# Kernel optimization log

Measured on AMD Instinct MI355X. Metric: run time of the kernel, lower is better.

## Reference

```python
import jax, jax.numpy as jnp
import numpy as np

C = 1.0          # Poincare ball curvature
NORM_FACTOR = 1.0
EPS = 1e-7
MAX_NORM = (1.0 - 1e-5) / np.sqrt(C)


def _artanh(x):
    x = jnp.clip(x, -1.0 + EPS, 1.0 - EPS)
    return jnp.arctanh(x)


def logmap0(x):
    # tangent vector at origin of Poincare ball (c=C)
    n = jnp.clip(jnp.linalg.norm(x, axis=-1, keepdims=True), EPS, None)
    sc = np.sqrt(C)
    return _artanh(sc * n) * x / (sc * n)


def expmap0(u):
    n = jnp.clip(jnp.linalg.norm(u, axis=-1, keepdims=True), EPS, None)
    sc = np.sqrt(C)
    return jnp.tanh(sc * n) * u / (sc * n)


def proj(x):
    # clip points to stay strictly inside the ball
    n = jnp.clip(jnp.linalg.norm(x, axis=-1, keepdims=True), EPS, None)
    return jnp.where(n > MAX_NORM, x / n * MAX_NORM, x)


def setup_inputs() -> dict:
    key = jax.random.key(0)
    ks = jax.random.split(key, 10)
    B, N, D_IN, D_H, D_LAT, L = 32, 1024, 128, 128, 64, 2
    s_in = 1.0 / np.sqrt(D_IN)
    s_h = 1.0 / np.sqrt(D_H)
    return {
        "node_features": jax.random.normal(ks[0], (B, N, D_IN), jnp.float32),
        "adjacency_matrix": jax.random.uniform(ks[1], (B, N, N), jnp.float32),
        "node_mask": jnp.ones((B, N, 1), jnp.float32),
        "W_embed": jax.random.normal(ks[2], (D_H, D_IN), jnp.float32) * s_in,
        "W_msg": jax.random.normal(ks[3], (L, D_H, D_H), jnp.float32) * s_h,
        "b_msg": jnp.zeros((L, D_H), jnp.float32),
        "W_agg": jax.random.normal(ks[4], (L, D_H, D_H), jnp.float32) * s_h,
        "b_agg": jnp.zeros((L, D_H), jnp.float32),
        "W_proj": jax.random.normal(ks[5], (2 * D_LAT, D_H), jnp.float32) * s_h,
        "b_proj": jnp.zeros((2 * D_LAT,), jnp.float32),
    }


def reference(node_features, adjacency_matrix, node_mask,
              W_embed, W_msg, b_msg, W_agg, b_agg, W_proj, b_proj):
    # feature embedding (bias-free linear, weights live on the manifold);
    # map to the Poincare ball
    h = jnp.einsum('bnd,hd->bnh', node_features, W_embed)
    x = proj(expmap0(h))

    num_layers = W_msg.shape[0]
    for l in range(num_layers):  # small fixed layer count
        t = logmap0(x)                                   # [B,N,D]
        m = t @ W_msg[l] + b_msg[l]                      # message transform
        agg = jnp.einsum('bij,bjd->bid', adjacency_matrix, m) / NORM_FACTOR
        agg = agg @ W_agg[l] + b_agg[l]                  # aggregation transform
        t = jax.nn.relu(m + agg)                         # tangent-space activation
        x = proj(expmap0(t))

    tangent = logmap0(x)                                 # final logmap0 in encode()
    mean_logvar = tangent @ W_proj.T + b_proj            # [B,N,2*latent]
    return mean_logvar * node_mask
```

## Files before the change

### kernel.cpp

```cpp
#include <hip/hip_runtime.h>
#include <hip/hip_bf16.h>

typedef __bf16 bf16;
typedef __bf16 bf16x8 __attribute__((ext_vector_type(8)));
typedef float  floatx4 __attribute__((ext_vector_type(4)));

#define EPSF    1e-7f
#define MAXNORM 0.99999f
#define TS_LD   136

__device__ __forceinline__ float hyp_scale(float ss) {
    float n  = sqrtf(ss);
    float nh = fmaxf(n, EPSF);
    float s1 = tanhf(nh) / nh;
    float nx = s1 * n;
    if (nx > MAXNORM) { s1 *= MAXNORM / nx; nx = MAXNORM; }
    float nx2 = fmaxf(nx, EPSF);
    return (atanhf(nx2) / nx2) * s1;
}

__device__ __forceinline__ bf16x8 cvt8(float4 a, float4 b) {
    bf16x8 r;
    r[0] = (bf16)a.x; r[1] = (bf16)a.y; r[2] = (bf16)a.z; r[3] = (bf16)a.w;
    r[4] = (bf16)b.x; r[5] = (bf16)b.y; r[6] = (bf16)b.z; r[7] = (bf16)b.w;
    return r;
}

__device__ __forceinline__ int sw128(int row, int k) {
    return row * 128 + (((k >> 3) ^ (row & 15)) << 3) + (k & 7);
}
__device__ __forceinline__ int sw64(int row, int k) {
    return row * 64 + (((k >> 3) ^ (row & 7)) << 3) + (k & 7);
}

__global__ __launch_bounds__(256) void embed_msg(
    const float* __restrict__ X, const float* __restrict__ Wemb,
    const float* __restrict__ Wmsg, const float* __restrict__ bmsg,
    bf16* __restrict__ M, bf16* __restrict__ MT)
{
    __shared__ __align__(16) bf16 Xs[128 * 128];
    __shared__ __align__(16) bf16 Ws[128 * 128];
    __shared__ __align__(16) bf16 W2[128 * 128];
    __shared__ __align__(16) bf16 Ts[128 * TS_LD];
    const int tid = threadIdx.x, bx = blockIdx.x;

    {
        const float4* Xg = reinterpret_cast<const float4*>(X + (size_t)bx * 16384);
        #pragma unroll
        for (int i = 0; i < 8; ++i) {
            int g = tid + i * 256, row = g >> 4, gc = g & 15;
            float4 v0 = Xg[2 * g], v1 = Xg[2 * g + 1];
            *reinterpret_cast<bf16x8*>(&Xs[row * 128 + ((gc ^ (row & 15)) << 3)]) = cvt8(v0, v1);
        }
    }
    {
        const float4* Wg = reinterpret_cast<const float4*>(Wemb);
        #pragma unroll
        for (int i = 0; i < 8; ++i) {
            int g = tid + i * 256, row = g >> 4, gc = g & 15;
            float4 v0 = Wg[2 * g], v1 = Wg[2 * g + 1];
            *reinterpret_cast<bf16x8*>(&Ws[row * 128 + ((gc ^ (row & 15)) << 3)]) = cvt8(v0, v1);
        }
    }
    {
        const int c0 = (tid & 15) * 8;
        #pragma unroll
        for (int rr = 0; rr < 8; ++rr) {
            int r = (tid >> 4) * 8 + rr;
            const float4* p = reinterpret_cast<const float4*>(Wmsg + r * 128 + c0);
            float4 v0 = p[0], v1 = p[1];
            float vv[8] = {v0.x, v0.y, v0.z, v0.w, v1.x, v1.y, v1.z, v1.w};
            #pragma unroll
            for (int j = 0; j < 8; ++j) {
                int n = c0 + j;
                W2[n * 128 + (((r >> 3) ^ (n & 15)) << 3) + (r & 7)] = (bf16)vv[j];
            }
        }
    }
    __syncthreads();

    const int lane = tid & 63, wv = tid >> 6, n16 = lane & 15, quad = lane >> 4;
    const int rbase = wv * 32;

    floatx4 acc[2][8];
    #pragma unroll
    for (int a = 0; a < 2; ++a)
        #pragma unroll
        for (int c = 0; c < 8; ++c) acc[a][c] = (floatx4){0.f, 0.f, 0.f, 0.f};
    #pragma unroll
    for (int kc = 0; kc < 4; ++kc) {
        int k0 = kc * 32 + quad * 8;
        bf16x8 a0 = *reinterpret_cast<const bf16x8*>(&Xs[sw128(rbase + n16, k0)]);
        bf16x8 a1 = *reinterpret_cast<const bf16x8*>(&Xs[sw128(rbase + 16 + n16, k0)]);
        #pragma unroll
        for (int ct = 0; ct < 8; ++ct) {
            bf16x8 b = *reinterpret_cast<const bf16x8*>(&Ws[sw128(ct * 16 + n16, k0)]);
            acc[0][ct] = __builtin_amdgcn_mfma_f32_16x16x32_bf16(a0, b, acc[0][ct], 0, 0, 0);
            acc[1][ct] = __builtin_amdgcn_mfma_f32_16x16x32_bf16(a1, b, acc[1][ct], 0, 0, 0);
        }
    }
    #pragma unroll
    for (int rt = 0; rt < 2; ++rt) {
        #pragma unroll
        for (int r = 0; r < 4; ++r) {
            int row = rbase + rt * 16 + quad * 4 + r;
            float u[8], ss = 0.f;
            #pragma unroll
            for (int ct = 0; ct < 8; ++ct) { u[ct] = acc[rt][ct][r]; ss += u[ct] * u[ct]; }
            #pragma unroll
            for (int off = 1; off < 16; off <<= 1) ss += __shfl_xor(ss, off);
            float sc = hyp_scale(ss);
            #pragma unroll
            for (int ct = 0; ct < 8; ++ct)
                Ts[row * TS_LD + ct * 16 + n16] = (bf16)(u[ct] * sc);
        }
    }
    __syncthreads();

    floatx4 acc2[2][8];
    #pragma unroll
    for (int a = 0; a < 2; ++a)
        #pragma unroll
        for (int c = 0; c < 8; ++c) acc2[a][c] = (floatx4){0.f, 0.f, 0.f, 0.f};
    #pragma unroll
    for (int kc = 0; kc < 4; ++kc) {
        int k0 = kc * 32 + quad * 8;
        bf16x8 a0 = *reinterpret_cast<const bf16x8*>(&Ts[(rbase + n16) * TS_LD + k0]);
        bf16x8 a1 = *reinterpret_cast<const bf16x8*>(&Ts[(rbase + 16 + n16) * TS_LD + k0]);
        #pragma unroll
        for (int ct = 0; ct < 8; ++ct) {
            bf16x8 b = *reinterpret_cast<const bf16x8*>(&W2[sw128(ct * 16 + n16, k0)]);
            acc2[0][ct] = __builtin_amdgcn_mfma_f32_16x16x32_bf16(a0, b, acc2[0][ct], 0, 0, 0);
            acc2[1][ct] = __builtin_amdgcn_mfma_f32_16x16x32_bf16(a1, b, acc2[1][ct], 0, 0, 0);
        }
    }
    float bv[8];
    #pragma unroll
    for (int ct = 0; ct < 8; ++ct) bv[ct] = bmsg[ct * 16 + n16];
    #pragma unroll
    for (int rt = 0; rt < 2; ++rt) {
        #pragma unroll
        for (int r = 0; r < 4; ++r) {
            int lrow = rbase + rt * 16 + quad * 4 + r;
            size_t grow = (size_t)bx * 128 + lrow;
            #pragma unroll
            for (int ct = 0; ct < 8; ++ct) {
                bf16 o = (bf16)(acc2[rt][ct][r] + bv[ct]);
                M[grow * 128 + ct * 16 + n16] = o;
                MT[((grow >> 10) * 128 + ct * 16 + n16) * 1024 + (grow & 1023)] = o;
            }
        }
    }
}

template <int LAST>
__global__ __launch_bounds__(512) void adj_fused(
    const float* __restrict__ Adj, const bf16* __restrict__ MT,
    const bf16* __restrict__ Mprev,
    const float* __restrict__ Wagg, const float* __restrict__ bagg,
    const float* __restrict__ W2f,  const float* __restrict__ b2,
    const float* __restrict__ Mask,
    bf16* __restrict__ Mout, bf16* __restrict__ MTout, float* __restrict__ Out)
{
    __shared__ __align__(16) bf16 smem[4 * 128 * 64];
    __shared__ __align__(16) bf16 Ts[128 * TS_LD];
    bf16* As0 = smem;
    bf16* As1 = smem + 128 * 64;
    bf16* Bs0 = smem + 2 * 128 * 64;
    bf16* Bs1 = smem + 3 * 128 * 64;

    const int tid = threadIdx.x, bid = blockIdx.x;
    const int mt = bid >> 5, b = bid & 31;
    const float* Ag = Adj + ((size_t)b << 20) + ((size_t)mt << 17);
    const bf16*  Bg = MT  + ((size_t)b << 17);

    const int lane = tid & 63, wv = tid >> 6, n16 = lane & 15, quad = lane >> 4;
    const int wr = (wv >> 2) * 64, wc = (wv & 3) * 32;

    const int kk0 = (bid * 5 + (bid >> 5)) & 15;

    floatx4 acc[4][2];
    #pragma unroll
    for (int a = 0; a < 4; ++a)
        #pragma unroll
        for (int c = 0; c < 2; ++c) acc[a][c] = (floatx4){0.f, 0.f, 0.f, 0.f};

    float4 pa[2][2]; bf16x8 pb[2];
    auto load_regs = [&](int kk) {
        #pragma unroll
        for (int i = 0; i < 2; ++i) {
            int g = tid + i * 512, row = g >> 3, gc = g & 7;
            const float4* pA = reinterpret_cast<const float4*>(
                Ag + (size_t)row * 1024 + kk * 64 + gc * 8);
            pa[i][0] = pA[0]; pa[i][1] = pA[1];
            pb[i] = *reinterpret_cast<const bf16x8*>(Bg + (size_t)row * 1024 + kk * 64 + gc * 8);
        }
    };
    auto store_lds = [&](bf16* A, bf16* B) {
        #pragma unroll
        for (int i = 0; i < 2; ++i) {
            int g = tid + i * 512, row = g >> 3, gc = g & 7;
            *reinterpret_cast<bf16x8*>(&A[row * 64 + ((gc ^ (row & 7)) << 3)]) = cvt8(pa[i][0], pa[i][1]);
            *reinterpret_cast<bf16x8*>(&B[row * 64 + ((gc ^ (row & 7)) << 3)]) = pb[i];
        }
    };

    load_regs(kk0);
    store_lds(As0, Bs0);
    for (int p = 0; p < 16; ++p) {
        bf16* Acur = (p & 1) ? As1 : As0;
        bf16* Bcur = (p & 1) ? Bs1 : Bs0;
        bf16* Anxt = (p & 1) ? As0 : As1;
        bf16* Bnxt = (p & 1) ? Bs0 : Bs1;
        __syncthreads();
        if (p < 15) load_regs((p + 1 + kk0) & 15);
        #pragma unroll
        for (int kc = 0; kc < 2; ++kc) {
            int ko = kc * 32 + quad * 8;
            bf16x8 a[4], bb[2];
            #pragma unroll
            for (int rt = 0; rt < 4; ++rt)
                a[rt] = *reinterpret_cast<const bf16x8*>(&Acur[sw64(wr + rt * 16 + n16, ko)]);
            #pragma unroll
            for (int ct = 0; ct < 2; ++ct)
                bb[ct] = *reinterpret_cast<const bf16x8*>(&Bcur[sw64(wc + ct * 16 + n16, ko)]);
            #pragma unroll
            for (int rt = 0; rt < 4; ++rt)
                #pragma unroll
                for (int ct = 0; ct < 2; ++ct)
                    acc[rt][ct] = __builtin_amdgcn_mfma_f32_16x16x32_bf16(a[rt], bb[ct], acc[rt][ct], 0, 0, 0);
        }
        if (p < 15) store_lds(Anxt, Bnxt);
    }
    __syncthreads();

    #pragma unroll
    for (int rt = 0; rt < 4; ++rt)
        #pragma unroll
        for (int ct = 0; ct < 2; ++ct)
            #pragma unroll
            for (int r = 0; r < 4; ++r) {
                int row = wr + rt * 16 + quad * 4 + r, col = wc + ct * 16 + n16;
                Ts[row * TS_LD + col] = (bf16)acc[rt][ct][r];
            }

    bf16* Wa = smem;
    bf16* W2 = smem + 128 * 128;
    {
        const int c0 = (tid & 15) * 8;
        #pragma unroll
        for (int rr = 0; rr < 4; ++rr) {
            int r = (tid >> 4) * 4 + rr;
            const float4* p = reinterpret_cast<const float4*>(Wagg + r * 128 + c0);
            float4 v0 = p[0], v1 = p[1];
            float vv[8] = {v0.x, v0.y, v0.z, v0.w, v1.x, v1.y, v1.z, v1.w};
            #pragma unroll
            for (int j = 0; j < 8; ++j) {
                int n = c0 + j;
                Wa[n * 128 + (((r >> 3) ^ (n & 15)) << 3) + (r & 7)] = (bf16)vv[j];
            }
        }
    }
    if (LAST) {
        const float4* Wg = reinterpret_cast<const float4*>(W2f);
        #pragma unroll
        for (int i = 0; i < 4; ++i) {
            int g = tid + i * 512, row = g >> 4, gc = g & 15;
            float4 v0 = Wg[2 * g], v1 = Wg[2 * g + 1];
            *reinterpret_cast<bf16x8*>(&W2[row * 128 + ((gc ^ (row & 15)) << 3)]) = cvt8(v0, v1);
        }
    } else {
        const int c0 = (tid & 15) * 8;
        #pragma unroll
        for (int rr = 0; rr < 4; ++rr) {
            int r = (tid >> 4) * 4 + rr;
            const float4* p = reinterpret_cast<const float4*>(W2f + r * 128 + c0);
            float4 v0 = p[0], v1 = p[1];
            float vv[8] = {v0.x, v0.y, v0.z, v0.w, v1.x, v1.y, v1.z, v1.w};
            #pragma unroll
            for (int j = 0; j < 8; ++j) {
                int n = c0 + j;
                W2[n * 128 + (((r >> 3) ^ (n & 15)) << 3) + (r & 7)] = (bf16)vv[j];
            }
        }
    }
    __syncthreads();

    const int rbase = wv * 16;
    const size_t growbase = (size_t)b * 1024 + (size_t)mt * 128;
    floatx4 acc2[8];
    #pragma unroll
    for (int c = 0; c < 8; ++c) acc2[c] = (floatx4){0.f, 0.f, 0.f, 0.f};
    #pragma unroll
    for (int kc = 0; kc < 4; ++kc) {
        int k0 = kc * 32 + quad * 8;
        bf16x8 a = *reinterpret_cast<const bf16x8*>(&Ts[(rbase + n16) * TS_LD + k0]);
        #pragma unroll
        for (int ct = 0; ct < 8; ++ct) {
            bf16x8 bb = *reinterpret_cast<const bf16x8*>(&Wa[sw128(ct * 16 + n16, k0)]);
            acc2[ct] = __builtin_amdgcn_mfma_f32_16x16x32_bf16(a, bb, acc2[ct], 0, 0, 0);
        }
    }
    {
        float bva[8];
        #pragma unroll
        for (int ct = 0; ct < 8; ++ct) bva[ct] = bagg[ct * 16 + n16];
        #pragma unroll
        for (int r = 0; r < 4; ++r) {
            int row = rbase + quad * 4 + r;
            size_t grow = growbase + row;
            float u[8], ss = 0.f;
            #pragma unroll
            for (int ct = 0; ct < 8; ++ct) {
                u[ct] = fmaxf(acc2[ct][r] + bva[ct] + (float)Mprev[grow * 128 + ct * 16 + n16], 0.f);
                ss += u[ct] * u[ct];
            }
            #pragma unroll
            for (int off = 1; off < 16; off <<= 1) ss += __shfl_xor(ss, off);
            float sc = hyp_scale(ss);
            #pragma unroll
            for (int ct = 0; ct < 8; ++ct)
                Ts[row * TS_LD + ct * 16 + n16] = (bf16)(u[ct] * sc);
        }
    }

    floatx4 acc3[8];
    #pragma unroll
    for (int c = 0; c < 8; ++c) acc3[c] = (floatx4){0.f, 0.f, 0.f, 0.f};
    #pragma unroll
    for (int kc = 0; kc < 4; ++kc) {
        int k0 = kc * 32 + quad * 8;
        bf16x8 a = *reinterpret_cast<const bf16x8*>(&Ts[(rbase + n16) * TS_LD + k0]);
        #pragma unroll
        for (int ct = 0; ct < 8; ++ct) {
            bf16x8 bb = *reinterpret_cast<const bf16x8*>(&W2[sw128(ct * 16 + n16, k0)]);
            acc3[ct] = __builtin_amdgcn_mfma_f32_16x16x32_bf16(a, bb, acc3[ct], 0, 0, 0);
        }
    }
    float bv2[8];
    #pragma unroll
    for (int ct = 0; ct < 8; ++ct) bv2[ct] = b2[ct * 16 + n16];
    #pragma unroll
    for (int r = 0; r < 4; ++r) {
        int row = rbase + quad * 4 + r;
        size_t grow = growbase + row;
        if (LAST) {
            float mk = Mask[grow];
            #pragma unroll
            for (int ct = 0; ct < 8; ++ct)
                Out[grow * 128 + ct * 16 + n16] = (acc3[ct][r] + bv2[ct]) * mk;
        } else {
            #pragma unroll
            for (int ct = 0; ct < 8; ++ct) {
                bf16 o = (bf16)(acc3[ct][r] + bv2[ct]);
                Mout[grow * 128 + ct * 16 + n16] = o;
                MTout[((grow >> 10) * 128 + ct * 16 + n16) * 1024 + (grow & 1023)] = o;
            }
        }
    }
}

extern "C" void kernel_launch(void* const* d_in, const int* in_sizes, int n_in,
                              void* d_out, int out_size, void* d_ws, size_t ws_size,
                              hipStream_t stream)
{
    const float* X    = (const float*)d_in[0];
    const float* Adj  = (const float*)d_in[1];
    const float* Mask = (const float*)d_in[2];
    const float* Wemb = (const float*)d_in[3];
    const float* Wmsg = (const float*)d_in[4];
    const float* bmsg = (const float*)d_in[5];
    const float* Wagg = (const float*)d_in[6];
    const float* bagg = (const float*)d_in[7];
    const float* Wprj = (const float*)d_in[8];
    const float* bprj = (const float*)d_in[9];
    float* out = (float*)d_out;

    const size_t BN = 32768;
    bf16* m0  = (bf16*)d_ws;
    bf16* m0T = m0  + BN * 128;
    bf16* m1  = m0T + BN * 128;
    bf16* m1T = m1  + BN * 128;

    embed_msg<<<256, 256, 0, stream>>>(X, Wemb, Wmsg, bmsg, m0, m0T);
    adj_fused<0><<<256, 512, 0, stream>>>(Adj, m0T, m0, Wagg, bagg,
                                          Wmsg + 16384, bmsg + 128, nullptr,
                                          m1, m1T, nullptr);
    adj_fused<1><<<256, 512, 0, stream>>>(Adj, m1T, m1, Wagg + 16384, bagg + 128,
                                          Wprj, bprj, Mask,
                                          nullptr, nullptr, out);
}
```

Baseline: 302.6 us.

## Pre-pack adjacency to swizzled bf16 and stream it via direct global-to-LDS loads

Adds a pack_adj kernel that converts the fp32 adjacency once into a tiled, pre-swizzled bf16 buffer in workspace. Both layer kernels then read it with global_load_lds in a three-stage pipeline, which avoids reading the fp32 adjacency twice and removes register-based conversion. The trade is an extra full fp32 read plus a bf16 write of the adjacency in the pack pass, and this path is taken only when the workspace is large enough; otherwise the old kernels run.

```diff
diff --git a/kernel.cpp b/kernel.cpp
--- a/kernel.cpp
+++ b/kernel.cpp
@@ -31,6 +31,27 @@
 }
 __device__ __forceinline__ int sw64(int row, int k) {
     return row * 64 + (((k >> 3) ^ (row & 7)) << 3) + (k & 7);
+}
+
+__device__ __forceinline__ void gl_lds16(const void* g, void* l) {
+    __builtin_amdgcn_global_load_lds(
+        (__attribute__((address_space(1))) unsigned int*)(g),
+        (__attribute__((address_space(3))) unsigned int*)(l), 16, 0, 0);
+}
+
+__global__ __launch_bounds__(256) void pack_adj(
+    const float* __restrict__ Adj, bf16* __restrict__ AdjB)
+{
+    const int t = threadIdx.x, bp = blockIdx.x;
+    #pragma unroll
+    for (int k = 0; k < 8; ++k) {
+        int G = bp * 2048 + k * 256 + t;
+        int gp = G & 7, row = (G >> 3) & 127, kk = (G >> 10) & 15, mtb = G >> 14;
+        const float4* s4 = reinterpret_cast<const float4*>(
+            Adj + ((size_t)mtb << 17) + (row << 10) + kk * 64 + ((gp ^ (row & 7)) << 3));
+        float4 v0 = s4[0], v1 = s4[1];
+        *reinterpret_cast<bf16x8*>(AdjB + (size_t)G * 8) = cvt8(v0, v1);
+    }
 }
 
 __global__ __launch_bounds__(256) void embed_msg(
@@ -148,6 +169,206 @@
                 bf16 o = (bf16)(acc2[rt][ct][r] + bv[ct]);
                 M[grow * 128 + ct * 16 + n16] = o;
                 MT[((grow >> 10) * 128 + ct * 16 + n16) * 1024 + (grow & 1023)] = o;
+            }
+        }
+    }
+}
+
+template <int LAST>
+__global__ __launch_bounds__(512) void adj_fast(
+    const bf16* __restrict__ AdjB, const bf16* __restrict__ MT,
+    const bf16* __restrict__ Mprev,
+    const float* __restrict__ Wagg, const float* __restrict__ bagg,
+    const float* __restrict__ W2f,  const float* __restrict__ b2,
+    const float* __restrict__ Mask,
+    bf16* __restrict__ Mout, bf16* __restrict__ MTout, float* __restrict__ Out)
+{
+    __shared__ __align__(16) bf16 smem[6 * 128 * 64];
+    __shared__ __align__(16) bf16 Ts[128 * TS_LD];
+
+    const int tid = threadIdx.x, bid = blockIdx.x;
+    const int mt = bid >> 5, b = bid & 31;
+    const bf16* Ab = AdjB + ((size_t)(b * 8 + mt) << 17);
+    const bf16* Bg = MT + ((size_t)b << 17);
+
+    const int lane = tid & 63, wv = tid >> 6, n16 = lane & 15, quad = lane >> 4;
+    const int wr = (wv >> 2) * 64, wc = (wv & 3) * 32;
+
+    bf16* As[3] = { smem,         smem + 8192,  smem + 16384 };
+    bf16* Bs[3] = { smem + 24576, smem + 32768, smem + 40960 };
+
+    floatx4 acc[4][2];
+    #pragma unroll
+    for (int a = 0; a < 4; ++a)
+        #pragma unroll
+        for (int c = 0; c < 2; ++c) acc[a][c] = (floatx4){0.f, 0.f, 0.f, 0.f};
+
+    auto stage = [&](int kk, bf16* Adst, bf16* Bdst) {
+        const bf16* at = Ab + (size_t)kk * 8192;
+        #pragma unroll
+        for (int j = 0; j < 2; ++j) {
+            int base = wv * 128 + j * 64;
+            gl_lds16(at + (size_t)(base + lane) * 8, Adst + base * 8);
+            int gi = base + lane;
+            int n = gi >> 3, gp = gi & 7;
+            gl_lds16(Bg + (size_t)n * 1024 + kk * 64 + ((gp ^ (n & 7)) << 3),
+                     Bdst + base * 8);
+        }
+    };
+
+    stage(0, As[0], Bs[0]);
+    stage(1, As[1], Bs[1]);
+    #pragma unroll
+    for (int p = 0; p < 16; ++p) {
+        if (p < 15) asm volatile("s_waitcnt vmcnt(4)" ::: "memory");
+        else        asm volatile("s_waitcnt vmcnt(0)" ::: "memory");
+        __builtin_amdgcn_s_barrier();
+        __builtin_amdgcn_sched_barrier(0);
+        if (p + 2 < 16) stage(p + 2, As[(p + 2) % 3], Bs[(p + 2) % 3]);
+        const bf16* Acur = As[p % 3];
+        const bf16* Bcur = Bs[p % 3];
+        #pragma unroll
+        for (int kc = 0; kc < 2; ++kc) {
+            int ko = kc * 32 + quad * 8;
+            bf16x8 a[4], bb[2];
+            #pragma unroll
+            for (int rt = 0; rt < 4; ++rt)
+                a[rt] = *reinterpret_cast<const bf16x8*>(&Acur[sw64(wr + rt * 16 + n16, ko)]);
+            #pragma unroll
+            for (int ct = 0; ct < 2; ++ct)
+                bb[ct] = *reinterpret_cast<const bf16x8*>(&Bcur[sw64(wc + ct * 16 + n16, ko)]);
+            __builtin_amdgcn_s_setprio(1);
+            #pragma unroll
+            for (int rt = 0; rt < 4; ++rt)
+                #pragma unroll
+                for (int ct = 0; ct < 2; ++ct)
+                    acc[rt][ct] = __builtin_amdgcn_mfma_f32_16x16x32_bf16(a[rt], bb[ct], acc[rt][ct], 0, 0, 0);
+            __builtin_amdgcn_s_setprio(0);
+        }
+    }
+    __syncthreads();
+
+    #pragma unroll
+    for (int rt = 0; rt < 4; ++rt)
+        #pragma unroll
+        for (int ct = 0; ct < 2; ++ct)
+            #pragma unroll
+            for (int r = 0; r < 4; ++r) {
+                int row = wr + rt * 16 + quad * 4 + r, col = wc + ct * 16 + n16;
+                Ts[row * TS_LD + col] = (bf16)acc[rt][ct][r];
+            }
+
+    bf16* Wa = smem;
+    bf16* W2 = smem + 128 * 128;
+    {
+        const int c0 = (tid & 15) * 8;
+        #pragma unroll
+        for (int rr = 0; rr < 4; ++rr) {
+            int r = (tid >> 4) * 4 + rr;
+            const float4* p = reinterpret_cast<const float4*>(Wagg + r * 128 + c0);
+            float4 v0 = p[0], v1 = p[1];
+            float vv[8] = {v0.x, v0.y, v0.z, v0.w, v1.x, v1.y, v1.z, v1.w};
+            #pragma unroll
+            for (int j = 0; j < 8; ++j) {
+                int n = c0 + j;
+                Wa[n * 128 + (((r >> 3) ^ (n & 15)) << 3) + (r & 7)] = (bf16)vv[j];
+            }
+        }
+    }
+    if (LAST) {
+        const float4* Wg = reinterpret_cast<const float4*>(W2f);
+        #pragma unroll
+        for (int i = 0; i < 4; ++i) {
+            int g = tid + i * 512, row = g >> 4, gc = g & 15;
+            float4 v0 = Wg[2 * g], v1 = Wg[2 * g + 1];
+            *reinterpret_cast<bf16x8*>(&W2[row * 128 + ((gc ^ (row & 15)) << 3)]) = cvt8(v0, v1);
+        }
+    } else {
+        const int c0 = (tid & 15) * 8;
+        #pragma unroll
+        for (int rr = 0; rr < 4; ++rr) {
+            int r = (tid >> 4) * 4 + rr;
+            const float4* p = reinterpret_cast<const float4*>(W2f + r * 128 + c0);
+            float4 v0 = p[0], v1 = p[1];
+            float vv[8] = {v0.x, v0.y, v0.z, v0.w, v1.x, v1.y, v1.z, v1.w};
+            #pragma unroll
+            for (int j = 0; j < 8; ++j) {
+                int n = c0 + j;
+                W2[n * 128 + (((r >> 3) ^ (n & 15)) << 3) + (r & 7)] = (bf16)vv[j];
+            }
+        }
+    }
+    __syncthreads();
+
+    const int rbase = wv * 16;
+    const size_t growbase = (size_t)b * 1024 + (size_t)mt * 128;
+    floatx4 acc2[8];
+    #pragma unroll
+    for (int c = 0; c < 8; ++c) acc2[c] = (floatx4){0.f, 0.f, 0.f, 0.f};
+    #pragma unroll
+    for (int kc = 0; kc < 4; ++kc) {
+        int k0 = kc * 32 + quad * 8;
+        bf16x8 a = *reinterpret_cast<const bf16x8*>(&Ts[(rbase + n16) * TS_LD + k0]);
+        #pragma unroll
+        for (int ct = 0; ct < 8; ++ct) {
+            bf16x8 bb = *reinterpret_cast<const bf16x8*>(&Wa[sw128(ct * 16 + n16, k0)]);
+            acc2[ct] = __builtin_amdgcn_mfma_f32_16x16x32_bf16(a, bb, acc2[ct], 0, 0, 0);
+        }
+    }
+    {
+        float bva[8];
+        #pragma unroll
+        for (int ct = 0; ct < 8; ++ct) bva[ct] = bagg[ct * 16 + n16];
+        #pragma unroll
+        for (int r = 0; r < 4; ++r) {
+            int row = rbase + quad * 4 + r;
+            size_t grow = growbase + row;
+            float u[8], ss = 0.f;
+            #pragma unroll
+            for (int ct = 0; ct < 8; ++ct) {
+                u[ct] = fmaxf(acc2[ct][r] + bva[ct] + (float)Mprev[grow * 128 + ct * 16 + n16], 0.f);
+                ss += u[ct] * u[ct];
+            }
+            #pragma unroll
+            for (int off = 1; off < 16; off <<= 1) ss += __shfl_xor(ss, off);
+            float sc = hyp_scale(ss);
+            #pragma unroll
+            for (int ct = 0; ct < 8; ++ct)
+                Ts[row * TS_LD + ct * 16 + n16] = (bf16)(u[ct] * sc);
+        }
+    }
+
+    floatx4 acc3[8];
+    #pragma unroll
+    for (int c = 0; c < 8; ++c) acc3[c] = (floatx4){0.f, 0.f, 0.f, 0.f};
+    #pragma unroll
+    for (int kc = 0; kc < 4; ++kc) {
+        int k0 = kc * 32 + quad * 8;
+        bf16x8 a = *reinterpret_cast<const bf16x8*>(&Ts[(rbase + n16) * TS_LD + k0]);
+        #pragma unroll
+        for (int ct = 0; ct < 8; ++ct) {
+            bf16x8 bb = *reinterpret_cast<const bf16x8*>(&W2[sw128(ct * 16 + n16, k0)]);
+            acc3[ct] = __builtin_amdgcn_mfma_f32_16x16x32_bf16(a, bb, acc3[ct], 0, 0, 0);
+        }
+    }
+    float bv2[8];
+    #pragma unroll
+    for (int ct = 0; ct < 8; ++ct) bv2[ct] = b2[ct * 16 + n16];
+    #pragma unroll
+    for (int r = 0; r < 4; ++r) {
+        int row = rbase + quad * 4 + r;
+        size_t grow = growbase + row;
+        if (LAST) {
+            float mk = Mask[grow];
+            #pragma unroll
+            for (int ct = 0; ct < 8; ++ct)
+                Out[grow * 128 + ct * 16 + n16] = (acc3[ct][r] + bv2[ct]) * mk;
+        } else {
+            #pragma unroll
+            for (int ct = 0; ct < 8; ++ct) {
+                bf16 o = (bf16)(acc3[ct][r] + bv2[ct]);
+                Mout[grow * 128 + ct * 16 + n16] = o;
+                MTout[((grow >> 10) * 128 + ct * 16 + n16) * 1024 + (grow & 1023)] = o;
             }
         }
     }
@@ -377,16 +598,30 @@
     float* out = (float*)d_out;
 
     const size_t BN = 32768;
-    bf16* m0  = (bf16*)d_ws;
-    bf16* m0T = m0  + BN * 128;
-    bf16* m1  = m0T + BN * 128;
-    bf16* m1T = m1  + BN * 128;
-
-    embed_msg<<<256, 256, 0, stream>>>(X, Wemb, Wmsg, bmsg, m0, m0T);
-    adj_fused<0><<<256, 512, 0, stream>>>(Adj, m0T, m0, Wagg, bagg,
-                                          Wmsg + 16384, bmsg + 128, nullptr,
-                                          m1, m1T, nullptr);
-    adj_fused<1><<<256, 512, 0, stream>>>(Adj, m1T, m1, Wagg + 16384, bagg + 128,
-                                          Wprj, bprj, Mask,
-                                          nullptr, nullptr, out);
-}
+    bf16* m0   = (bf16*)d_ws;
+    bf16* m0T  = m0  + BN * 128;
+    bf16* m1   = m0T + BN * 128;
+    bf16* m1T  = m1  + BN * 128;
+    bf16* AdjB = m1T + BN * 128;
+
+    const size_t need = (4 * BN * 128 + (size_t)33554432) * sizeof(bf16);
+
+    if (ws_size >= need) {
+        pack_adj<<<2048, 256, 0, stream>>>(Adj, AdjB);
+        embed_msg<<<256, 256, 0, stream>>>(X, Wemb, Wmsg, bmsg, m0, m0T);
+        adj_fast<0><<<256, 512, 0, stream>>>(AdjB, m0T, m0, Wagg, bagg,
+                                             Wmsg + 16384, bmsg + 128, nullptr,
+                                             m1, m1T, nullptr);
+        adj_fast<1><<<256, 512, 0, stream>>>(AdjB, m1T, m1, Wagg + 16384, bagg + 128,
+                                             Wprj, bprj, Mask,
+                                             nullptr, nullptr, out);
+    } else {
+        embed_msg<<<256, 256, 0, stream>>>(X, Wemb, Wmsg, bmsg, m0, m0T);
+        adj_fused<0><<<256, 512, 0, stream>>>(Adj, m0T, m0, Wagg, bagg,
+                                              Wmsg + 16384, bmsg + 128, nullptr,
+                                              m1, m1T, nullptr);
+        adj_fused<1><<<256, 512, 0, stream>>>(Adj, m1T, m1, Wagg + 16384, bagg + 128,
+                                              Wprj, bprj, Mask,
+                                              nullptr, nullptr, out);
+    }
+}
```

Measured after the change: 317.2 us. 4.8% more time.

## Pre-tile transposed messages, stage B via direct global-to-LDS loads, double grid

Applied to the files above, without the earlier changes.

Messages are now written to MT in a pre-tiled, pre-swizzled 64-column block layout, staged through LDS so the global stores are coalesced 16-byte vectors instead of scattered 2-byte transposed writes. The adjacency kernel then copies B tiles straight into LDS with global_load_lds, skipping the register round trip. Each block now covers 64 rows instead of 128, so the grid doubles to 512 blocks for better CU occupancy on a memory-bound adjacency stream. In exchange, the B tiles are loaded twice as often across blocks, and half the waves sit idle during the small dense epilogue GEMMs.

```diff
diff --git a/kernel.cpp b/kernel.cpp
--- a/kernel.cpp
+++ b/kernel.cpp
@@ -32,6 +32,13 @@
 __device__ __forceinline__ int sw64(int row, int k) {
     return row * 64 + (((k >> 3) ^ (row & 7)) << 3) + (k & 7);
 }
+
+__device__ __forceinline__ void gl_lds16(const void* g, void* l) {
+    __builtin_amdgcn_global_load_lds(
+        (__attribute__((address_space(1))) unsigned int*)(g),
+        (__attribute__((address_space(3))) unsigned int*)(l), 16, 0, 0);
+}
+
 
 __global__ __launch_bounds__(256) void embed_msg(
     const float* __restrict__ X, const float* __restrict__ Wemb,
@@ -144,17 +151,39 @@
             int lrow = rbase + rt * 16 + quad * 4 + r;
             size_t grow = (size_t)bx * 128 + lrow;
             #pragma unroll
+            for (int ct = 0; ct < 8; ++ct)
+                M[grow * 128 + ct * 16 + n16] = (bf16)(acc2[rt][ct][r] + bv[ct]);
+        }
+    }
+    __syncthreads();
+    bf16* Ts2 = W2;
+    #pragma unroll
+    for (int rt = 0; rt < 2; ++rt) {
+        #pragma unroll
+        for (int r = 0; r < 4; ++r) {
+            int lrow = rbase + rt * 16 + quad * 4 + r;
+            #pragma unroll
             for (int ct = 0; ct < 8; ++ct) {
-                bf16 o = (bf16)(acc2[rt][ct][r] + bv[ct]);
-                M[grow * 128 + ct * 16 + n16] = o;
-                MT[((grow >> 10) * 128 + ct * 16 + n16) * 1024 + (grow & 1023)] = o;
-            }
+                int dim = ct * 16 + n16;
+                Ts2[dim * 128 + (lrow ^ ((dim & 7) << 3))] = (bf16)(acc2[rt][ct][r] + bv[ct]);
+            }
+        }
+    }
+    __syncthreads();
+    {
+        const size_t tb = (((size_t)(bx >> 3) * 16 + (size_t)(bx & 7) * 2) << 10);
+        #pragma unroll
+        for (int i = 0; i < 8; ++i) {
+            int g = i * 256 + tid;
+            int gp = g & 7, n = (g >> 3) & 127, kkl = g >> 10;
+            bf16x8 v = *reinterpret_cast<const bf16x8*>(&Ts2[n * 128 + kkl * 64 + gp * 8]);
+            *reinterpret_cast<bf16x8*>(MT + ((tb + (size_t)g) << 3)) = v;
         }
     }
 }
 
 template <int LAST>
-__global__ __launch_bounds__(512) void adj_fused(
+__global__ __launch_bounds__(512) void adj_fast(
     const float* __restrict__ Adj, const bf16* __restrict__ MT,
     const bf16* __restrict__ Mprev,
     const float* __restrict__ Wagg, const float* __restrict__ bagg,
@@ -162,80 +191,84 @@
     const float* __restrict__ Mask,
     bf16* __restrict__ Mout, bf16* __restrict__ MTout, float* __restrict__ Out)
 {
-    __shared__ __align__(16) bf16 smem[4 * 128 * 64];
-    __shared__ __align__(16) bf16 Ts[128 * TS_LD];
-    bf16* As0 = smem;
-    bf16* As1 = smem + 128 * 64;
-    bf16* Bs0 = smem + 2 * 128 * 64;
-    bf16* Bs1 = smem + 3 * 128 * 64;
+    __shared__ __align__(16) bf16 smem[33280];
 
     const int tid = threadIdx.x, bid = blockIdx.x;
-    const int mt = bid >> 5, b = bid & 31;
-    const float* Ag = Adj + ((size_t)b << 20) + ((size_t)mt << 17);
-    const bf16*  Bg = MT  + ((size_t)b << 17);
+    const int h = bid >> 8, inner = bid & 255;
+    const int mt = inner >> 5, b = inner & 31;
+    const float* Ag = Adj + ((size_t)b << 20) + ((size_t)mt << 17) + ((size_t)h << 16);
+    const bf16*  Bg = MT + ((size_t)b << 17);
 
     const int lane = tid & 63, wv = tid >> 6, n16 = lane & 15, quad = lane >> 4;
-    const int wr = (wv >> 2) * 64, wc = (wv & 3) * 32;
+    const int wr = (wv >> 2) * 32, wc = (wv & 3) * 32;
 
     const int kk0 = (bid * 5 + (bid >> 5)) & 15;
 
-    floatx4 acc[4][2];
-    #pragma unroll
-    for (int a = 0; a < 4; ++a)
+    floatx4 acc[2][2];
+    #pragma unroll
+    for (int a = 0; a < 2; ++a)
         #pragma unroll
         for (int c = 0; c < 2; ++c) acc[a][c] = (floatx4){0.f, 0.f, 0.f, 0.f};
 
-    float4 pa[2][2]; bf16x8 pb[2];
+    const int arow = tid >> 3, agc = tid & 7;
+    float4 pa0, pa1;
     auto load_regs = [&](int kk) {
-        #pragma unroll
-        for (int i = 0; i < 2; ++i) {
-            int g = tid + i * 512, row = g >> 3, gc = g & 7;
-            const float4* pA = reinterpret_cast<const float4*>(
-                Ag + (size_t)row * 1024 + kk * 64 + gc * 8);
-            pa[i][0] = pA[0]; pa[i][1] = pA[1];
-            pb[i] = *reinterpret_cast<const bf16x8*>(Bg + (size_t)row * 1024 + kk * 64 + gc * 8);
-        }
+        const float4* pA = reinterpret_cast<const float4*>(
+            Ag + (size_t)arow * 1024 + kk * 64 + agc * 8);
+        pa0 = pA[0]; pa1 = pA[1];
     };
-    auto store_lds = [&](bf16* A, bf16* B) {
-        #pragma unroll
-        for (int i = 0; i < 2; ++i) {
-            int g = tid + i * 512, row = g >> 3, gc = g & 7;
-            *reinterpret_cast<bf16x8*>(&A[row * 64 + ((gc ^ (row & 7)) << 3)]) = cvt8(pa[i][0], pa[i][1]);
-            *reinterpret_cast<bf16x8*>(&B[row * 64 + ((gc ^ (row & 7)) << 3)]) = pb[i];
-        }
+    auto store_lds = [&](int slot) {
+        bf16* A = smem + slot * 4096;
+        *reinterpret_cast<bf16x8*>(&A[arow * 64 + ((agc ^ (arow & 7)) << 3)]) = cvt8(pa0, pa1);
     };
+    auto stage_b = [&](int kk, int slot) {
+        const bf16* bt = Bg + ((size_t)kk << 13);
+        bf16* Bdst = smem + 8192 + slot * 8192;
+        #pragma unroll
+        for (int j = 0; j < 2; ++j) {
+            int base = wv * 128 + j * 64;
+            gl_lds16(bt + (size_t)(base + lane) * 8, Bdst + base * 8);
+        }
+    };
 
     load_regs(kk0);
-    store_lds(As0, Bs0);
+    stage_b(kk0, 0);
+    store_lds(0);
     for (int p = 0; p < 16; ++p) {
-        bf16* Acur = (p & 1) ? As1 : As0;
-        bf16* Bcur = (p & 1) ? Bs1 : Bs0;
-        bf16* Anxt = (p & 1) ? As0 : As1;
-        bf16* Bnxt = (p & 1) ? Bs0 : Bs1;
+        const bf16* Acur = smem + (p & 1) * 4096;
+        const bf16* Bcur = smem + 8192 + (p & 1) * 8192;
         __syncthreads();
-        if (p < 15) load_regs((p + 1 + kk0) & 15);
+        if (p < 15) {
+            int nk = (p + 1 + kk0) & 15;
+            load_regs(nk);
+            stage_b(nk, (p + 1) & 1);
+        }
         #pragma unroll
         for (int kc = 0; kc < 2; ++kc) {
             int ko = kc * 32 + quad * 8;
-            bf16x8 a[4], bb[2];
-            #pragma unroll
-            for (int rt = 0; rt < 4; ++rt)
+            bf16x8 a[2], bb[2];
+            #pragma unroll
+            for (int rt = 0; rt < 2; ++rt)
                 a[rt] = *reinterpret_cast<const bf16x8*>(&Acur[sw64(wr + rt * 16 + n16, ko)]);
             #pragma unroll
             for (int ct = 0; ct < 2; ++ct)
                 bb[ct] = *reinterpret_cast<const bf16x8*>(&Bcur[sw64(wc + ct * 16 + n16, ko)]);
             #pragma unroll
-            for (int rt = 0; rt < 4; ++rt)
+            for (int rt = 0; rt < 2; ++rt)
                 #pragma unroll
                 for (int ct = 0; ct < 2; ++ct)
                     acc[rt][ct] = __builtin_amdgcn_mfma_f32_16x16x32_bf16(a[rt], bb[ct], acc[rt][ct], 0, 0, 0);
         }
-        if (p < 15) store_lds(Anxt, Bnxt);
-    }
-    __syncthreads();
-
-    #pragma unroll
-    for (int rt = 0; rt < 4; ++rt)
+        if (p < 15) store_lds((p + 1) & 1);
+    }
+    __syncthreads();
+
+    bf16* Ts  = smem;
+    bf16* Wa  = smem + 8704;
+    bf16* Ts2 = smem + 25088;
+
+    #pragma unroll
+    for (int rt = 0; rt < 2; ++rt)
         #pragma unroll
         for (int ct = 0; ct < 2; ++ct)
             #pragma unroll
@@ -243,9 +276,6 @@
                 int row = wr + rt * 16 + quad * 4 + r, col = wc + ct * 16 + n16;
                 Ts[row * TS_LD + col] = (bf16)acc[rt][ct][r];
             }
-
-    bf16* Wa = smem;
-    bf16* W2 = smem + 128 * 128;
     {
         const int c0 = (tid & 15) * 8;
         #pragma unroll
@@ -261,13 +291,54 @@
             }
         }
     }
+    __syncthreads();
+
+    const int rbase = (wv & 3) * 16;
+    const size_t growbase = (size_t)b * 1024 + (size_t)mt * 128 + (size_t)h * 64;
+    floatx4 acc2[8];
+    #pragma unroll
+    for (int c = 0; c < 8; ++c) acc2[c] = (floatx4){0.f, 0.f, 0.f, 0.f};
+    if (wv < 4) {
+        #pragma unroll
+        for (int kc = 0; kc < 4; ++kc) {
+            int k0 = kc * 32 + quad * 8;
+            bf16x8 a = *reinterpret_cast<const bf16x8*>(&Ts[(rbase + n16) * TS_LD + k0]);
+            #pragma unroll
+            for (int ct = 0; ct < 8; ++ct) {
+                bf16x8 bb = *reinterpret_cast<const bf16x8*>(&Wa[sw128(ct * 16 + n16, k0)]);
+                acc2[ct] = __builtin_amdgcn_mfma_f32_16x16x32_bf16(a, bb, acc2[ct], 0, 0, 0);
+            }
+        }
+        float bva[8];
+        #pragma unroll
+        for (int ct = 0; ct < 8; ++ct) bva[ct] = bagg[ct * 16 + n16];
+        #pragma unroll
+        for (int r = 0; r < 4; ++r) {
+            int row = rbase + quad * 4 + r;
+            size_t grow = growbase + row;
+            float u[8], ss = 0.f;
+            #pragma unroll
+            for (int ct = 0; ct < 8; ++ct) {
+                u[ct] = fmaxf(acc2[ct][r] + bva[ct] + (float)Mprev[grow * 128 + ct * 16 + n16], 0.f);
+                ss += u[ct] * u[ct];
+            }
+            #pragma unroll
+            for (int off = 1; off < 16; off <<= 1) ss += __shfl_xor(ss, off);
+            float sc = hyp_scale(ss);
+            #pragma unroll
+            for (int ct = 0; ct < 8; ++ct)
+                Ts[row * TS_LD + ct * 16 + n16] = (bf16)(u[ct] * sc);
+        }
+    }
+    __syncthreads();
+
     if (LAST) {
         const float4* Wg = reinterpret_cast<const float4*>(W2f);
         #pragma unroll
         for (int i = 0; i < 4; ++i) {
             int g = tid + i * 512, row = g >> 4, gc = g & 15;
             float4 v0 = Wg[2 * g], v1 = Wg[2 * g + 1];
-            *reinterpret_cast<bf16x8*>(&W2[row * 128 + ((gc ^ (row & 15)) << 3)]) = cvt8(v0, v1);
+            *reinterpret_cast<bf16x8*>(&Wa[row * 128 + ((gc ^ (row & 15)) << 3)]) = cvt8(v0, v1);
         }
     } else {
         const int c0 = (tid & 15) * 8;
@@ -280,82 +351,58 @@
             #pragma unroll
             for (int j = 0; j < 8; ++j) {
                 int n = c0 + j;
-                W2[n * 128 + (((r >> 3) ^ (n & 15)) << 3) + (r & 7)] = (bf16)vv[j];
-            }
-        }
-    }
-    __syncthreads();
-
-    const int rbase = wv * 16;
-    const size_t growbase = (size_t)b * 1024 + (size_t)mt * 128;
-    floatx4 acc2[8];
-    #pragma unroll
-    for (int c = 0; c < 8; ++c) acc2[c] = (floatx4){0.f, 0.f, 0.f, 0.f};
-    #pragma unroll
-    for (int kc = 0; kc < 4; ++kc) {
-        int k0 = kc * 32 + quad * 8;
-        bf16x8 a = *reinterpret_cast<const bf16x8*>(&Ts[(rbase + n16) * TS_LD + k0]);
-        #pragma unroll
-        for (int ct = 0; ct < 8; ++ct) {
-            bf16x8 bb = *reinterpret_cast<const bf16x8*>(&Wa[sw128(ct * 16 + n16, k0)]);
-            acc2[ct] = __builtin_amdgcn_mfma_f32_16x16x32_bf16(a, bb, acc2[ct], 0, 0, 0);
-        }
-    }
-    {
-        float bva[8];
-        #pragma unroll
-        for (int ct = 0; ct < 8; ++ct) bva[ct] = bagg[ct * 16 + n16];
+                Wa[n * 128 + (((r >> 3) ^ (n & 15)) << 3) + (r & 7)] = (bf16)vv[j];
+            }
+        }
+    }
+    __syncthreads();
+
+    floatx4 acc3[8];
+    #pragma unroll
+    for (int c = 0; c < 8; ++c) acc3[c] = (floatx4){0.f, 0.f, 0.f, 0.f};
+    if (wv < 4) {
+        #pragma unroll
+        for (int kc = 0; kc < 4; ++kc) {
+            int k0 = kc * 32 + quad * 8;
+            bf16x8 a = *reinterpret_cast<const bf16x8*>(&Ts[(rbase + n16) * TS_LD + k0]);
+            #pragma unroll
+            for (int ct = 0; ct < 8; ++ct) {
+                bf16x8 bb = *reinterpret_cast<const bf16x8*>(&Wa[sw128(ct * 16 + n16, k0)]);
+                acc3[ct] = __builtin_amdgcn_mfma_f32_16x16x32_bf16(a, bb, acc3[ct], 0, 0, 0);
+            }
+        }
+        float bv2[8];
+        #pragma unroll
+        for (int ct = 0; ct < 8; ++ct) bv2[ct] = b2[ct * 16 + n16];
         #pragma unroll
         for (int r = 0; r < 4; ++r) {
             int row = rbase + quad * 4 + r;
             size_t grow = growbase + row;
-            float u[8], ss = 0.f;
-            #pragma unroll
-            for (int ct = 0; ct < 8; ++ct) {
-                u[ct] = fmaxf(acc2[ct][r] + bva[ct] + (float)Mprev[grow * 128 + ct * 16 + n16], 0.f);
-                ss += u[ct] * u[ct];
-            }
-            #pragma unroll
-            for (int off = 1; off < 16; off <<= 1) ss += __shfl_xor(ss, off);
-            float sc = hyp_scale(ss);
-            #pragma unroll
-            for (int ct = 0; ct < 8; ++ct)
-                Ts[row * TS_LD + ct * 16 + n16] = (bf16)(u[ct] * sc);
-        }
-    }
-
-    floatx4 acc3[8];
-    #pragma unroll
-    for (int c = 0; c < 8; ++c) acc3[c] = (floatx4){0.f, 0.f, 0.f, 0.f};
-    #pragma unroll
-    for (int kc = 0; kc < 4; ++kc) {
-        int k0 = kc * 32 + quad * 8;
-        bf16x8 a = *reinterpret_cast<const bf16x8*>(&Ts[(rbase + n16) * TS_LD + k0]);
-        #pragma unroll
-        for (int ct = 0; ct < 8; ++ct) {
-            bf16x8 bb = *reinterpret_cast<const bf16x8*>(&W2[sw128(ct * 16 + n16, k0)]);
-            acc3[ct] = __builtin_amdgcn_mfma_f32_16x16x32_bf16(a, bb, acc3[ct], 0, 0, 0);
-        }
-    }
-    float bv2[8];
-    #pragma unroll
-    for (int ct = 0; ct < 8; ++ct) bv2[ct] = b2[ct * 16 + n16];
-    #pragma unroll
-    for (int r = 0; r < 4; ++r) {
-        int row = rbase + quad * 4 + r;
-        size_t grow = growbase + row;
-        if (LAST) {
-            float mk = Mask[grow];
-            #pragma unroll
-            for (int ct = 0; ct < 8; ++ct)
-                Out[grow * 128 + ct * 16 + n16] = (acc3[ct][r] + bv2[ct]) * mk;
-        } else {
-            #pragma unroll
-            for (int ct = 0; ct < 8; ++ct) {
-                bf16 o = (bf16)(acc3[ct][r] + bv2[ct]);
-                Mout[grow * 128 + ct * 16 + n16] = o;
-                MTout[((grow >> 10) * 128 + ct * 16 + n16) * 1024 + (grow & 1023)] = o;
-            }
+            if (LAST) {
+                float mk = Mask[grow];
+                #pragma unroll
+                for (int ct = 0; ct < 8; ++ct)
+                    Out[grow * 128 + ct * 16 + n16] = (acc3[ct][r] + bv2[ct]) * mk;
+            } else {
+                #pragma unroll
+                for (int ct = 0; ct < 8; ++ct) {
+                    int dim = ct * 16 + n16;
+                    bf16 o = (bf16)(acc3[ct][r] + bv2[ct]);
+                    Mout[grow * 128 + dim] = o;
+                    Ts2[dim * 64 + (row ^ ((dim & 7) << 3))] = o;
+                }
+            }
+        }
+    }
+    if (!LAST) {
+        __syncthreads();
+        const size_t tb = (((size_t)b * 16 + (size_t)(mt * 2 + h)) << 10);
+        #pragma unroll
+        for (int i = 0; i < 2; ++i) {
+            int g = i * 512 + tid;
+            int gp = g & 7, n = g >> 3;
+            bf16x8 v = *reinterpret_cast<const bf16x8*>(&Ts2[n * 64 + gp * 8]);
+            *reinterpret_cast<bf16x8*>(MTout + ((tb + (size_t)g) << 3)) = v;
         }
     }
 }
@@ -377,16 +424,16 @@
     float* out = (float*)d_out;
 
     const size_t BN = 32768;
-    bf16* m0  = (bf16*)d_ws;
-    bf16* m0T = m0  + BN * 128;
-    bf16* m1  = m0T + BN * 128;
-    bf16* m1T = m1  + BN * 128;
+    bf16* m0   = (bf16*)d_ws;
+    bf16* m0T  = m0  + BN * 128;
+    bf16* m1   = m0T + BN * 128;
+    bf16* m1T  = m1  + BN * 128;
 
     embed_msg<<<256, 256, 0, stream>>>(X, Wemb, Wmsg, bmsg, m0, m0T);
-    adj_fused<0><<<256, 512, 0, stream>>>(Adj, m0T, m0, Wagg, bagg,
-                                          Wmsg + 16384, bmsg + 128, nullptr,
-                                          m1, m1T, nullptr);
-    adj_fused<1><<<256, 512, 0, stream>>>(Adj, m1T, m1, Wagg + 16384, bagg + 128,
-                                          Wprj, bprj, Mask,
-                                          nullptr, nullptr, out);
-}
+    adj_fast<0><<<512, 512, 0, stream>>>(Adj, m0T, m0, Wagg, bagg,
+                                         Wmsg + 16384, bmsg + 128, nullptr,
+                                         m1, m1T, nullptr);
+    adj_fast<1><<<512, 512, 0, stream>>>(Adj, m1T, m1, Wagg + 16384, bagg + 128,
+                                         Wprj, bprj, Mask,
+                                         nullptr, nullptr, out);
+}
```

Result: no change. 300.8 us (-0.6%).
